# Performance work log

Hardware: AMD Instinct MI355X
Metric: run time of the kernel (lower is better)

## Reference

```python
import jax, jax.numpy as jnp
import numpy as np

N_NODES = 50000
N_EDGES = 500000
H = 128
C = 2


def setup_inputs() -> dict:
    key = jax.random.key(0)
    ks = jax.random.split(key, 8)
    node_repr = jax.random.normal(ks[0], (N_NODES, H), dtype=jnp.float32)
    src = jax.random.randint(ks[1], (N_EDGES,), 0, N_NODES, dtype=jnp.int32)
    dst = jax.random.randint(ks[2], (N_EDGES,), 0, N_NODES, dtype=jnp.int32)
    # Linear weights stored as (in, out); scaled like torch default init
    W1 = jax.random.normal(ks[3], (4 * H, 2 * H), dtype=jnp.float32) / np.sqrt(4 * H)
    b1 = jnp.zeros((2 * H,), dtype=jnp.float32)
    W2 = jax.random.normal(ks[4], (2 * H, H), dtype=jnp.float32) / np.sqrt(2 * H)
    b2 = jnp.zeros((H,), dtype=jnp.float32)
    W3 = jax.random.normal(ks[5], (H, C), dtype=jnp.float32) / np.sqrt(H)
    b3 = jnp.zeros((C,), dtype=jnp.float32)
    return {"node_repr": node_repr, "src": src, "dst": dst,
            "W1": W1, "b1": b1, "W2": W2, "b2": b2, "W3": W3, "b3": b3}


def reference(node_repr, src, dst, W1, b1, W2, b2, W3, b3):
    h_i = node_repr[src]                      # [E, H] gather
    h_j = node_repr[dst]                      # [E, H] gather
    diff = jnp.abs(h_i - h_j)
    product = h_i * h_j
    edge_input = jnp.concatenate([h_i, h_j, diff, product], axis=1)  # [E, 4H]
    x = jax.nn.relu(edge_input @ W1 + b1)     # [E, 2H]; dropout = identity (eval)
    x = jax.nn.relu(x @ W2 + b2)              # [E, H]
    return x @ W3 + b3                        # [E, C]
```

## Files before the change

kernel.cpp:

```cpp
#include <hip/hip_runtime.h>


#define H 128

typedef __bf16 bf16x8 __attribute__((ext_vector_type(8)));
typedef float f32x4 __attribute__((ext_vector_type(4)));

__device__ __forceinline__ unsigned short f2bf(float f) {
    unsigned u = __builtin_bit_cast(unsigned, f);
    u += 0x7FFFu + ((u >> 16) & 1u);
    return (unsigned short)(u >> 16);
}
__device__ __forceinline__ float bfhi(unsigned u) {
    return __builtin_bit_cast(float, u & 0xffff0000u);
}
__device__ __forceinline__ float bflo(unsigned u) {
    return __builtin_bit_cast(float, u << 16);
}
__device__ __forceinline__ void comb2(unsigned ua, unsigned ub,
                                      unsigned& dd, unsigned& pp) {
    float a0 = bflo(ua), a1 = bfhi(ua);
    float b0 = bflo(ub), b1 = bfhi(ub);
    float d0 = a0 - b0, d1 = a1 - b1;
    float p0 = a0 * b0, p1 = a1 * b1;
    unsigned rd, rp;
    asm("v_cvt_pk_bf16_f32 %0, |%1|, |%2|" : "=v"(rd) : "v"(d0), "v"(d1));
    asm("v_cvt_pk_bf16_f32 %0, %1, %2" : "=v"(rp) : "v"(p0), "v"(p1));
    dd = rd; pp = rp;
}
__device__ __forceinline__ unsigned pkbf(float v0, float v1) {
    unsigned r;
    asm("v_cvt_pk_bf16_f32 %0, %1, %2" : "=v"(r) : "v"(v0), "v"(v1));
    return r;
}

__global__ void prep_node(const float* __restrict__ node, unsigned short* __restrict__ nbf) {
    int idx = blockIdx.x * 256 + threadIdx.x;
    const f32x4* p = (const f32x4*)(node) + idx;
    f32x4 v = *p;
    ushort4 w;
    w.x = f2bf(v.x); w.y = f2bf(v.y); w.z = f2bf(v.z); w.w = f2bf(v.w);
    *(ushort4*)(nbf + idx * 4) = w;
}

__global__ void prep_w1(const float* __restrict__ W1, unsigned short* __restrict__ W1P) {
    int o = blockIdx.x * 256 + threadIdx.x;
    int chunk = o >> 9;
    int g_nt = chunk >> 4;
    int ks = chunk & 15;
    int r = o & 511;
    int lane = r >> 3;
    int j = r & 7;
    int row = g_nt * 16 + (lane & 15);
    int k = ks * 32 + (lane >> 4) * 8 + j;
    W1P[o] = f2bf(W1[k * 256 + row]);
}

__global__ void prep_w2(const float* __restrict__ W2, unsigned short* __restrict__ W2P) {
    int o = blockIdx.x * 256 + threadIdx.x;
    int chunk = o >> 9;
    int g_nt = chunk >> 3;
    int ks = chunk & 7;
    int r = o & 511;
    int lane = r >> 3;
    int j = r & 7;
    int row = g_nt * 16 + (lane & 15);
    int k = ks * 32 + (lane >> 4) * 8 + j;
    W2P[o] = f2bf(W2[k * 128 + row]);
}

__launch_bounds__(256, 4)
__global__ void fused_mlp(const unsigned short* __restrict__ nbf,
                          const int* __restrict__ src,
                          const int* __restrict__ dst,
                          const unsigned short* __restrict__ W1P,
                          const float* __restrict__ b1,
                          const unsigned short* __restrict__ W2P,
                          const float* __restrict__ b2,
                          const float* __restrict__ W3,
                          const float* __restrict__ b3,
                          float* __restrict__ out,
                          int E) {
    __shared__ __align__(16) unsigned short sH[64 * 268];
    __shared__ __align__(16) float sW3[256];

    const int t = threadIdx.x;
    const int e0 = blockIdx.x * 64;

    const int lane = t & 63;
    const int wv = t >> 6;
    const int quad = lane >> 4;
    const int lrow = lane & 15;
    const int nb = wv * 64;
    const int nb2 = wv * 32;

    const unsigned short* w1b = W1P + wv * 32768 + lane * 8;
    const unsigned short* w2b = W2P + wv * 8192 + lane * 8;

    {
        int r = t >> 2;
        int q = t & 3;
        int e = e0 + r;
        int ec = e < E ? e : (E - 1);
        const unsigned short* hi = nbf + (long)src[ec] * H + q * 32;
        const unsigned short* hj = nbf + (long)dst[ec] * H + q * 32;
        unsigned short* rowp = sH + r * 268 + q * 32;
#pragma unroll
        for (int b = 0; b < 4; b++) {
            uint4 a = *(const uint4*)(hi + b * 8);
            uint4 c = *(const uint4*)(hj + b * 8);
            *(uint4*)(rowp + b * 8)       = a;
            *(uint4*)(rowp + 136 + b * 8) = c;
        }
        sW3[(t & 1) * 128 + (t >> 1)] = W3[t];
    }
    __syncthreads();

    f32x4 acc[4][4];
#pragma unroll
    for (int mt = 0; mt < 4; mt++)
#pragma unroll
        for (int nt = 0; nt < 4; nt++)
            acc[mt][nt] = (f32x4){0.f, 0.f, 0.f, 0.f};

    int aoff[4];
#pragma unroll
    for (int mt = 0; mt < 4; mt++) aoff[mt] = (mt * 16 + lrow) * 268 + quad * 8;

#pragma unroll 1
    for (int ks = 0; ks < 8; ks++) {
        const int ao = (ks < 4) ? ks * 32 : 136 + (ks - 4) * 32;
        bf16x8 bv[4], av[4];
#pragma unroll
        for (int nt = 0; nt < 4; nt++) bv[nt] = *(const bf16x8*)(w1b + nt * 8192 + ks * 512);
#pragma unroll
        for (int mt = 0; mt < 4; mt++) av[mt] = *(const bf16x8*)(sH + aoff[mt] + ao);
#pragma unroll
        for (int mt = 0; mt < 4; mt++)
#pragma unroll
            for (int nt = 0; nt < 4; nt++)
                acc[mt][nt] = __builtin_amdgcn_mfma_f32_16x16x32_bf16(av[mt], bv[nt], acc[mt][nt], 0, 0, 0);
    }

#pragma unroll 1
    for (int ks = 0; ks < 4; ks++) {
        bf16x8 avd[4], avp[4];
#pragma unroll
        for (int mt = 0; mt < 4; mt++) {
            uint4 hu = *(const uint4*)(sH + aoff[mt] + ks * 32);
            uint4 ju = *(const uint4*)(sH + aoff[mt] + 136 + ks * 32);
            uint4 cd, cp;
            comb2(hu.x, ju.x, cd.x, cp.x);
            comb2(hu.y, ju.y, cd.y, cp.y);
            comb2(hu.z, ju.z, cd.z, cp.z);
            comb2(hu.w, ju.w, cd.w, cp.w);
            avd[mt] = __builtin_bit_cast(bf16x8, cd);
            avp[mt] = __builtin_bit_cast(bf16x8, cp);
        }
#pragma unroll
        for (int nt = 0; nt < 4; nt++) {
            bf16x8 bvd = *(const bf16x8*)(w1b + nt * 8192 + (ks + 8) * 512);
            bf16x8 bvp = *(const bf16x8*)(w1b + nt * 8192 + (ks + 12) * 512);
#pragma unroll
            for (int mt = 0; mt < 4; mt++) {
                acc[mt][nt] = __builtin_amdgcn_mfma_f32_16x16x32_bf16(avd[mt], bvd, acc[mt][nt], 0, 0, 0);
                acc[mt][nt] = __builtin_amdgcn_mfma_f32_16x16x32_bf16(avp[mt], bvp, acc[mt][nt], 0, 0, 0);
            }
        }
    }

    float b1v[4];
#pragma unroll
    for (int nt = 0; nt < 4; nt++) b1v[nt] = b1[nb + nt * 16 + lrow];
    float b2v[2];
#pragma unroll
    for (int nt = 0; nt < 2; nt++) b2v[nt] = b2[nb2 + nt * 16 + lrow];

    __syncthreads();
    unsigned short* sx1 = sH;
#pragma unroll
    for (int mt = 0; mt < 4; mt++)
#pragma unroll
        for (int nt = 0; nt < 4; nt++) {
            float v0 = acc[mt][nt][0] + b1v[nt]; v0 = v0 > 0.f ? v0 : 0.f;
            float v1 = acc[mt][nt][1] + b1v[nt]; v1 = v1 > 0.f ? v1 : 0.f;
            float v2 = acc[mt][nt][2] + b1v[nt]; v2 = v2 > 0.f ? v2 : 0.f;
            float v3 = acc[mt][nt][3] + b1v[nt]; v3 = v3 > 0.f ? v3 : 0.f;
            unsigned r01 = pkbf(v0, v1);
            unsigned r23 = pkbf(v2, v3);
            unsigned short* base = sx1 + (mt * 16 + quad * 4) * 268 + nb + nt * 16 + lrow;
            base[0]   = (unsigned short)r01;
            base[268] = (unsigned short)(r01 >> 16);
            base[536] = (unsigned short)r23;
            base[804] = (unsigned short)(r23 >> 16);
        }
    __syncthreads();

    f32x4 acc2[4][2];
#pragma unroll
    for (int mt = 0; mt < 4; mt++)
#pragma unroll
        for (int nt = 0; nt < 2; nt++)
            acc2[mt][nt] = (f32x4){0.f, 0.f, 0.f, 0.f};

#pragma unroll 1
    for (int ks = 0; ks < 8; ks++) {
        bf16x8 bv2[2], av2[4];
#pragma unroll
        for (int nt = 0; nt < 2; nt++) bv2[nt] = *(const bf16x8*)(w2b + nt * 4096 + ks * 512);
#pragma unroll
        for (int mt = 0; mt < 4; mt++) av2[mt] = *(const bf16x8*)(sx1 + aoff[mt] + ks * 32);
#pragma unroll
        for (int mt = 0; mt < 4; mt++)
#pragma unroll
            for (int nt = 0; nt < 2; nt++)
                acc2[mt][nt] = __builtin_amdgcn_mfma_f32_16x16x32_bf16(av2[mt], bv2[nt], acc2[mt][nt], 0, 0, 0);
    }

    __syncthreads();
    unsigned short* sx2 = sH;
#pragma unroll
    for (int mt = 0; mt < 4; mt++)
#pragma unroll
        for (int nt = 0; nt < 2; nt++) {
            float v0 = acc2[mt][nt][0] + b2v[nt]; v0 = v0 > 0.f ? v0 : 0.f;
            float v1 = acc2[mt][nt][1] + b2v[nt]; v1 = v1 > 0.f ? v1 : 0.f;
            float v2 = acc2[mt][nt][2] + b2v[nt]; v2 = v2 > 0.f ? v2 : 0.f;
            float v3 = acc2[mt][nt][3] + b2v[nt]; v3 = v3 > 0.f ? v3 : 0.f;
            unsigned r01 = pkbf(v0, v1);
            unsigned r23 = pkbf(v2, v3);
            unsigned short* base = sx2 + (mt * 16 + quad * 4) * 140 + nb2 + nt * 16 + lrow;
            base[0]   = (unsigned short)r01;
            base[140] = (unsigned short)(r01 >> 16);
            base[280] = (unsigned short)r23;
            base[420] = (unsigned short)(r23 >> 16);
        }
    __syncthreads();

    {
        int r = t >> 2;
        int c = t & 1;
        int h = (t >> 1) & 1;
        const unsigned short* xr = sx2 + r * 140 + h * 64;
        const float* w3c = sW3 + c * 128 + h * 64;
        float s = 0.f;
#pragma unroll
        for (int j = 0; j < 8; j++) {
            uint4 v = *(const uint4*)(xr + j * 8);
            f32x4 w0 = *(const f32x4*)(w3c + j * 8);
            f32x4 w1 = *(const f32x4*)(w3c + j * 8 + 4);
            s += bflo(v.x) * w0[0] + bfhi(v.x) * w0[1]
               + bflo(v.y) * w0[2] + bfhi(v.y) * w0[3]
               + bflo(v.z) * w1[0] + bfhi(v.z) * w1[1]
               + bflo(v.w) * w1[2] + bfhi(v.w) * w1[3];
        }
        s += __shfl_xor(s, 2);
        int e = e0 + r;
        if (h == 0 && e < E) out[e * 2 + c] = s + b3[c];
    }
}

extern "C" void kernel_launch(void* const* d_in, const int* in_sizes, int n_in,
                              void* d_out, int out_size, void* d_ws, size_t ws_size,
                              hipStream_t stream) {
    const float* node = (const float*)d_in[0];
    const int* src    = (const int*)d_in[1];
    const int* dst    = (const int*)d_in[2];
    const float* W1   = (const float*)d_in[3];
    const float* b1   = (const float*)d_in[4];
    const float* W2   = (const float*)d_in[5];
    const float* b2   = (const float*)d_in[6];
    const float* W3   = (const float*)d_in[7];
    const float* b3   = (const float*)d_in[8];
    float* out = (float*)d_out;
    const int NN = in_sizes[0] / H;
    const int E = in_sizes[1];

    unsigned short* W1P = (unsigned short*)d_ws;
    unsigned short* W2P = W1P + 512 * 256;
    unsigned short* NBF = W2P + 256 * 128;

    hipLaunchKernelGGL(prep_node, dim3((NN * H / 4 + 255) / 256), dim3(256), 0, stream, node, NBF);
    hipLaunchKernelGGL(prep_w1, dim3(512), dim3(256), 0, stream, W1, W1P);
    hipLaunchKernelGGL(prep_w2, dim3(128), dim3(256), 0, stream, W2, W2P);
    const int nblk = (E + 63) / 64;
    hipLaunchKernelGGL(fused_mlp, dim3(nblk), dim3(256), 0, stream,
                       NBF, src, dst, W1P, b1, W2P, b2, W3, b3, out, E);
}
```

Before: 337.0 us.

## Drop node bf16 prepass; gather fp32 rows and convert in-kernel, merge weight preps

Removes the separate kernel that converted the whole node table to bf16. The fused MLP kernel now gathers fp32 rows directly and packs them to bf16 while staging into shared memory. The two weight-packing kernels are merged into one launch to cut launch overhead. The trade-off is that each gather reads twice as many bytes per edge (about 1M row gathers), in exchange for skipping a full read and write pass over the 25 MB node table.

```diff
diff --git a/kernel.cpp b/kernel.cpp
--- a/kernel.cpp
+++ b/kernel.cpp
@@ -34,43 +34,35 @@
     return r;
 }
 
-__global__ void prep_node(const float* __restrict__ node, unsigned short* __restrict__ nbf) {
-    int idx = blockIdx.x * 256 + threadIdx.x;
-    const f32x4* p = (const f32x4*)(node) + idx;
-    f32x4 v = *p;
-    ushort4 w;
-    w.x = f2bf(v.x); w.y = f2bf(v.y); w.z = f2bf(v.z); w.w = f2bf(v.w);
-    *(ushort4*)(nbf + idx * 4) = w;
-}
-
-__global__ void prep_w1(const float* __restrict__ W1, unsigned short* __restrict__ W1P) {
-    int o = blockIdx.x * 256 + threadIdx.x;
-    int chunk = o >> 9;
-    int g_nt = chunk >> 4;
-    int ks = chunk & 15;
-    int r = o & 511;
-    int lane = r >> 3;
-    int j = r & 7;
-    int row = g_nt * 16 + (lane & 15);
-    int k = ks * 32 + (lane >> 4) * 8 + j;
-    W1P[o] = f2bf(W1[k * 256 + row]);
-}
-
-__global__ void prep_w2(const float* __restrict__ W2, unsigned short* __restrict__ W2P) {
-    int o = blockIdx.x * 256 + threadIdx.x;
-    int chunk = o >> 9;
-    int g_nt = chunk >> 3;
-    int ks = chunk & 7;
-    int r = o & 511;
-    int lane = r >> 3;
-    int j = r & 7;
-    int row = g_nt * 16 + (lane & 15);
-    int k = ks * 32 + (lane >> 4) * 8 + j;
-    W2P[o] = f2bf(W2[k * 128 + row]);
+__global__ void prep_w(const float* __restrict__ W1, const float* __restrict__ W2,
+                       unsigned short* __restrict__ W1P, unsigned short* __restrict__ W2P) {
+    if (blockIdx.x < 512) {
+        int o = blockIdx.x * 256 + threadIdx.x;
+        int chunk = o >> 9;
+        int g_nt = chunk >> 4;
+        int ks = chunk & 15;
+        int r = o & 511;
+        int lane = r >> 3;
+        int j = r & 7;
+        int row = g_nt * 16 + (lane & 15);
+        int k = ks * 32 + (lane >> 4) * 8 + j;
+        W1P[o] = f2bf(W1[k * 256 + row]);
+    } else {
+        int o = (blockIdx.x - 512) * 256 + threadIdx.x;
+        int chunk = o >> 9;
+        int g_nt = chunk >> 3;
+        int ks = chunk & 7;
+        int r = o & 511;
+        int lane = r >> 3;
+        int j = r & 7;
+        int row = g_nt * 16 + (lane & 15);
+        int k = ks * 32 + (lane >> 4) * 8 + j;
+        W2P[o] = f2bf(W2[k * 128 + row]);
+    }
 }
 
 __launch_bounds__(256, 4)
-__global__ void fused_mlp(const unsigned short* __restrict__ nbf,
+__global__ void fused_mlp(const float* __restrict__ node,
                           const int* __restrict__ src,
                           const int* __restrict__ dst,
                           const unsigned short* __restrict__ W1P,
@@ -102,13 +94,20 @@
         int q = t & 3;
         int e = e0 + r;
         int ec = e < E ? e : (E - 1);
-        const unsigned short* hi = nbf + (long)src[ec] * H + q * 32;
-        const unsigned short* hj = nbf + (long)dst[ec] * H + q * 32;
+        const float* hi = node + (long)src[ec] * H + q * 32;
+        const float* hj = node + (long)dst[ec] * H + q * 32;
         unsigned short* rowp = sH + r * 268 + q * 32;
 #pragma unroll
         for (int b = 0; b < 4; b++) {
-            uint4 a = *(const uint4*)(hi + b * 8);
-            uint4 c = *(const uint4*)(hj + b * 8);
+            f32x4 a0 = *(const f32x4*)(hi + b * 8);
+            f32x4 a1 = *(const f32x4*)(hi + b * 8 + 4);
+            f32x4 c0 = *(const f32x4*)(hj + b * 8);
+            f32x4 c1 = *(const f32x4*)(hj + b * 8 + 4);
+            uint4 a, c;
+            a.x = pkbf(a0[0], a0[1]); a.y = pkbf(a0[2], a0[3]);
+            a.z = pkbf(a1[0], a1[1]); a.w = pkbf(a1[2], a1[3]);
+            c.x = pkbf(c0[0], c0[1]); c.y = pkbf(c0[2], c0[3]);
+            c.z = pkbf(c1[0], c1[1]); c.w = pkbf(c1[2], c1[3]);
             *(uint4*)(rowp + b * 8)       = a;
             *(uint4*)(rowp + 136 + b * 8) = c;
         }
@@ -273,17 +272,13 @@
     const float* W3   = (const float*)d_in[7];
     const float* b3   = (const float*)d_in[8];
     float* out = (float*)d_out;
-    const int NN = in_sizes[0] / H;
     const int E = in_sizes[1];
 
     unsigned short* W1P = (unsigned short*)d_ws;
     unsigned short* W2P = W1P + 512 * 256;
-    unsigned short* NBF = W2P + 256 * 128;
-
-    hipLaunchKernelGGL(prep_node, dim3((NN * H / 4 + 255) / 256), dim3(256), 0, stream, node, NBF);
-    hipLaunchKernelGGL(prep_w1, dim3(512), dim3(256), 0, stream, W1, W1P);
-    hipLaunchKernelGGL(prep_w2, dim3(128), dim3(256), 0, stream, W2, W2P);
+
+    hipLaunchKernelGGL(prep_w, dim3(640), dim3(256), 0, stream, W1, W2, W1P, W2P);
     const int nblk = (E + 63) / 64;
     hipLaunchKernelGGL(fused_mlp, dim3(nblk), dim3(256), 0, stream,
-                       NBF, src, dst, W1P, b1, W2P, b2, W3, b3, out, E);
-}
+                       node, src, dst, W1P, b1, W2P, b2, W3, b3, out, E);
+}
```

After: 372.4 us. 1.11x slower.
